# Performance work log

Measured on AMD Instinct MI355X. Metric: run time of the kernel, lower is better.

The kernel has to match this reference:

```python
import jax, jax.numpy as jnp
import numpy as np

B, N, Mc, K = 8, 16384, 2048, 32
EMB = 256


def setup_inputs() -> dict:
    key = jax.random.key(0)
    ks = jax.random.split(key, 9)
    xyz = jax.random.normal(ks[0], (B, N, 3), dtype=jnp.float32)
    centers = jax.random.normal(ks[1], (B, Mc, 3), dtype=jnp.float32)
    idx_knn = jax.random.randint(ks[2], (B, Mc, K), 0, N, dtype=jnp.int32)
    # 1x1 conv weights == pointwise linear layers (out_ch, in_ch) + bias
    def kaiming(k, o, i):
        return jax.random.normal(k, (o, i), dtype=jnp.float32) * np.float32(np.sqrt(2.0 / i))
    W1, b1 = kaiming(ks[3], 64, 3), jnp.zeros((64,), jnp.float32)
    W2, b2 = kaiming(ks[4], 128, 64), jnp.zeros((128,), jnp.float32)
    W3, b3 = kaiming(ks[5], EMB, 128), jnp.zeros((EMB,), jnp.float32)
    return {"xyz": xyz, "centers": centers, "idx_knn": idx_knn,
            "W1": W1, "b1": b1, "W2": W2, "b2": b2, "W3": W3, "b3": b3}


def reference(xyz, centers, idx_knn, W1, b1, W2, b2, W3, b3):
    # gather KNN neighbors: (B, M, K, 3)
    neigh = jnp.take_along_axis(xyz[:, None, :, :], idx_knn[..., None], axis=2)
    local = neigh - centers[:, :, None, :]          # center-subtract
    # 1x1 convs are pointwise linears over the channel dim
    h = jax.nn.relu(jnp.einsum('bmkc,oc->bmko', local, W1) + b1)
    h = jax.nn.relu(jnp.einsum('bmkc,oc->bmko', h, W2) + b2)
    h = jnp.einsum('bmkc,oc->bmko', h, W3) + b3      # (B, M, K, EMB)
    return jnp.max(h, axis=2)                        # max over K -> (B, M, EMB)
```

## Files before the change

### kernel.cpp

```cpp
#include <hip/hip_runtime.h>
#include <hip/hip_bf16.h>


typedef __attribute__((ext_vector_type(8))) short bf16x8;
typedef __attribute__((ext_vector_type(4))) float f32x4v;

constexpr int Bn = 8, Nn = 16384, Mn = 2048, Kn = 32, EMB = 256;
constexpr int G = 2;
constexpr int ROWS = G * Kn;

__device__ __forceinline__ unsigned pk2(float a, float b) {
    float2 f; f.x = a; f.y = b;
    __hip_bfloat162 h = __float22bfloat162_rn(f);
    return *(unsigned*)&h;
}

__device__ __forceinline__ bf16x8 pack8(const float* v) {
    unsigned u0 = pk2(v[0], v[1]), u1 = pk2(v[2], v[3]);
    unsigned u2 = pk2(v[4], v[5]), u3 = pk2(v[6], v[7]);
    uint4 u = make_uint4(u0, u1, u2, u3);
    return *(bf16x8*)&u;
}

__global__ __launch_bounds__(256) void pe_pack(
    const float* __restrict__ W2, const float* __restrict__ W3,
    uint4* __restrict__ ws)
{
    int gid = blockIdx.x * 256 + threadIdx.x;
    if (gid < 1024) {
        int e = gid, l = e & 63;
        int kt = (e >> 6) & 1, ct = (e >> 7) & 1, w = e >> 8;
        int q = l >> 4, n = l & 15;
        int ch = w * 32 + ct * 16 + n;
        const float* p = W2 + ch * 64 + kt * 32 + q * 8;
        float t[8];
        *(float4*)&t[0] = *(const float4*)p;
        *(float4*)&t[4] = *(const float4*)(p + 4);
        bf16x8 v = pack8(t);
        ws[e] = *(uint4*)&v;
    } else if (gid < 5120) {
        int e = gid - 1024, l = e & 63;
        int kt = (e >> 6) & 3, ct = (e >> 8) & 3, w = e >> 10;
        int q = l >> 4, n = l & 15;
        int ch = w * 64 + ct * 16 + n;
        const float* p = W3 + ch * 128 + kt * 32 + q * 8;
        float t[8];
        *(float4*)&t[0] = *(const float4*)p;
        *(float4*)&t[4] = *(const float4*)(p + 4);
        bf16x8 v = pack8(t);
        ws[1024 + e] = *(uint4*)&v;
    }
}

__global__ __launch_bounds__(256, 4) void pe_mfma(
    const float* __restrict__ xyz,
    const float* __restrict__ centers,
    const int*   __restrict__ idx,
    const float* __restrict__ W1,
    const float* __restrict__ b1,
    const float* __restrict__ b2,
    const float* __restrict__ b3,
    const uint4* __restrict__ wsf,
    float*       __restrict__ out)
{
    __shared__ uint4 h1v[ROWS * 64 * 2 / 16];
    __shared__ uint4 h2v[ROWS * 128 * 2 / 16];

    const int tid = threadIdx.x;
    const int w   = tid >> 6;
    const int l   = tid & 63;
    const int q   = l >> 4;
    const int n   = l & 15;
    const int bm0 = blockIdx.x * G;

    bf16x8 B2f[2][2];
    float4 bb2[2];
    const int ch0 = w * 32 + q * 4;
    #pragma unroll
    for (int ct = 0; ct < 2; ++ct) {
        bb2[ct] = *(const float4*)&b2[ch0 + ct * 16];
        #pragma unroll
        for (int kt = 0; kt < 2; ++kt) {
            uint4 u = wsf[((w * 2 + ct) * 2 + kt) * 64 + l];
            B2f[ct][kt] = *(bf16x8*)&u;
        }
    }
    bf16x8 B3f[4][4];  float b3v[4];
    #pragma unroll
    for (int ct = 0; ct < 4; ++ct) {
        b3v[ct] = b3[w * 64 + ct * 16 + n];
        #pragma unroll
        for (int kt = 0; kt < 4; ++kt) {
            uint4 u = wsf[1024 + ((w * 4 + ct) * 4 + kt) * 64 + l];
            B3f[ct][kt] = *(bf16x8*)&u;
        }
    }

    const int r64 = tid & 63;
    {
        int bm = bm0 + (r64 >> 5);
        int bb = bm >> 11;
        int id = idx[(size_t)bm * Kn + (r64 & 31)];
        const float* p = xyz + ((size_t)bb * Nn + id) * 3;
        const float* c = centers + (size_t)bm * 3;
        float lx = p[0] - c[0], ly = p[1] - c[1], lz = p[2] - c[2];

        const int o4b = __builtin_amdgcn_readfirstlane((tid >> 6) * 4);
        float h[16];
        #pragma unroll
        for (int i = 0; i < 4; ++i) {
            const float4* Wp = (const float4*)(W1 + (o4b + i) * 12);
            float4 wa = Wp[0], wb = Wp[1], wc = Wp[2];
            float4 bb4 = *(const float4*)(b1 + (o4b + i) * 4);
            h[4*i+0] = fmaxf(bb4.x + lx*wa.x + ly*wa.y + lz*wa.z, 0.f);
            h[4*i+1] = fmaxf(bb4.y + lx*wa.w + ly*wb.x + lz*wb.y, 0.f);
            h[4*i+2] = fmaxf(bb4.z + lx*wb.z + ly*wb.w + lz*wc.x, 0.f);
            h[4*i+3] = fmaxf(bb4.w + lx*wc.y + ly*wc.z + lz*wc.w, 0.f);
        }
        const int T = r64 >> 4, r = r64 & 15, j0 = (tid >> 6) * 2;
        #pragma unroll
        for (int jj = 0; jj < 2; ++jj) {
            bf16x8 v = pack8(&h[8 * jj]);
            h1v[T * 128 + (j0 + jj) * 16 + r] = *(uint4*)&v;
        }
    }
    __syncthreads();

    {
        ushort* h2s = (ushort*)h2v;
        #pragma unroll
        for (int rt = 0; rt < G * 2; ++rt) {
            uint4 a0u = h1v[rt * 128 + q * 16 + n];
            uint4 a1u = h1v[rt * 128 + (4 + q) * 16 + n];
            bf16x8 A0 = *(bf16x8*)&a0u, A1 = *(bf16x8*)&a1u;
            #pragma unroll
            for (int ct = 0; ct < 2; ++ct) {
                int ch = ch0 + ct * 16;
                f32x4v c0 = {0.f, 0.f, 0.f, 0.f};
                c0 = __builtin_amdgcn_mfma_f32_16x16x32_bf16(B2f[ct][0], A0, c0, 0, 0, 0);
                c0 = __builtin_amdgcn_mfma_f32_16x16x32_bf16(B2f[ct][1], A1, c0, 0, 0, 0);
                unsigned p0 = pk2(fmaxf(c0[0] + bb2[ct].x, 0.f),
                                  fmaxf(c0[1] + bb2[ct].y, 0.f));
                unsigned p1 = pk2(fmaxf(c0[2] + bb2[ct].z, 0.f),
                                  fmaxf(c0[3] + bb2[ct].w, 0.f));
                uint2 pk; pk.x = p0; pk.y = p1;
                *(uint2*)&h2s[rt * 2048 + (ch >> 3) * 128 + n * 8 + (ch & 7)] = pk;
            }
        }
    }
    __syncthreads();

    {
        #pragma unroll
        for (int g = 0; g < G; ++g) {
            bf16x8 Ae[4], Ao[4];
            #pragma unroll
            for (int kt = 0; kt < 4; ++kt) {
                uint4 ae = h2v[(2*g)   * 256 + (kt * 4 + q) * 16 + n];
                uint4 ao = h2v[(2*g+1) * 256 + (kt * 4 + q) * 16 + n];
                Ae[kt] = *(bf16x8*)&ae;
                Ao[kt] = *(bf16x8*)&ao;
            }
            #pragma unroll
            for (int ct = 0; ct < 4; ++ct) {
                f32x4v Ce = {0.f, 0.f, 0.f, 0.f};
                f32x4v Co = {0.f, 0.f, 0.f, 0.f};
                #pragma unroll
                for (int kt = 0; kt < 4; ++kt) {
                    Ce = __builtin_amdgcn_mfma_f32_16x16x32_bf16(Ae[kt], B3f[ct][kt], Ce, 0, 0, 0);
                    Co = __builtin_amdgcn_mfma_f32_16x16x32_bf16(Ao[kt], B3f[ct][kt], Co, 0, 0, 0);
                }
                float v = fmaxf(fmaxf(fmaxf(Ce[0], Co[0]), fmaxf(Ce[1], Co[1])),
                                fmaxf(fmaxf(Ce[2], Co[2]), fmaxf(Ce[3], Co[3])));
                v = fmaxf(v, __shfl_xor(v, 16));
                v = fmaxf(v, __shfl_xor(v, 32));
                if (q == 0) {
                    out[(size_t)(bm0 + g) * EMB + w * 64 + ct * 16 + n] = v + b3v[ct];
                }
            }
        }
    }
}

extern "C" void kernel_launch(void* const* d_in, const int* in_sizes, int n_in,
                              void* d_out, int out_size, void* d_ws, size_t ws_size,
                              hipStream_t stream) {
    const float* xyz     = (const float*)d_in[0];
    const float* centers = (const float*)d_in[1];
    const int*   idx     = (const int*)  d_in[2];
    const float* W1      = (const float*)d_in[3];
    const float* b1      = (const float*)d_in[4];
    const float* W2      = (const float*)d_in[5];
    const float* b2      = (const float*)d_in[6];
    const float* W3      = (const float*)d_in[7];
    const float* b3      = (const float*)d_in[8];
    float*       out     = (float*)d_out;
    uint4*       ws      = (uint4*)d_ws;

    pe_pack<<<20, 256, 0, stream>>>(W2, W3, ws);
    pe_mfma<<<(Bn * Mn) / G, 256, 0, stream>>>(
        xyz, centers, idx, W1, b1, b2, b3, ws, out);
}
```

Baseline: 124.1 us.

## Stream W3 fragments from global inside loop to cut registers and raise occupancy

Stops preloading all 16 W3 MFMA B-fragments and the b3 values into registers at kernel start. Each output tile now loads its four fragments from the packed workspace inside a non-unrolled loop, and the launch bound is raised from 4 to 6 waves per SIMD. The goal is to lower VGPR pressure so more blocks stay resident and latency is hidden better. In exchange, W3 is reloaded from global/L2 for every group and channel tile, and serialized loops expose load latency before each MFMA chain.

```diff
diff --git a/kernel.cpp b/kernel.cpp
--- a/kernel.cpp
+++ b/kernel.cpp
@@ -52,7 +52,7 @@
     }
 }
 
-__global__ __launch_bounds__(256, 4) void pe_mfma(
+__global__ __launch_bounds__(256, 6) void pe_mfma(
     const float* __restrict__ xyz,
     const float* __restrict__ centers,
     const int*   __restrict__ idx,
@@ -83,16 +83,6 @@
         for (int kt = 0; kt < 2; ++kt) {
             uint4 u = wsf[((w * 2 + ct) * 2 + kt) * 64 + l];
             B2f[ct][kt] = *(bf16x8*)&u;
-        }
-    }
-    bf16x8 B3f[4][4];  float b3v[4];
-    #pragma unroll
-    for (int ct = 0; ct < 4; ++ct) {
-        b3v[ct] = b3[w * 64 + ct * 16 + n];
-        #pragma unroll
-        for (int kt = 0; kt < 4; ++kt) {
-            uint4 u = wsf[1024 + ((w * 4 + ct) * 4 + kt) * 64 + l];
-            B3f[ct][kt] = *(bf16x8*)&u;
         }
     }
 
@@ -151,7 +141,7 @@
     __syncthreads();
 
     {
-        #pragma unroll
+        #pragma unroll 1
         for (int g = 0; g < G; ++g) {
             bf16x8 Ae[4], Ao[4];
             #pragma unroll
@@ -161,21 +151,27 @@
                 Ae[kt] = *(bf16x8*)&ae;
                 Ao[kt] = *(bf16x8*)&ao;
             }
-            #pragma unroll
+            #pragma unroll 1
             for (int ct = 0; ct < 4; ++ct) {
+                const uint4* bp = &wsf[1024 + (w * 4 + ct) * 256 + l];
+                uint4 u0 = bp[0], u1 = bp[64], u2 = bp[128], u3 = bp[192];
                 f32x4v Ce = {0.f, 0.f, 0.f, 0.f};
                 f32x4v Co = {0.f, 0.f, 0.f, 0.f};
-                #pragma unroll
-                for (int kt = 0; kt < 4; ++kt) {
-                    Ce = __builtin_amdgcn_mfma_f32_16x16x32_bf16(Ae[kt], B3f[ct][kt], Ce, 0, 0, 0);
-                    Co = __builtin_amdgcn_mfma_f32_16x16x32_bf16(Ao[kt], B3f[ct][kt], Co, 0, 0, 0);
-                }
+                Ce = __builtin_amdgcn_mfma_f32_16x16x32_bf16(Ae[0], *(bf16x8*)&u0, Ce, 0, 0, 0);
+                Co = __builtin_amdgcn_mfma_f32_16x16x32_bf16(Ao[0], *(bf16x8*)&u0, Co, 0, 0, 0);
+                Ce = __builtin_amdgcn_mfma_f32_16x16x32_bf16(Ae[1], *(bf16x8*)&u1, Ce, 0, 0, 0);
+                Co = __builtin_amdgcn_mfma_f32_16x16x32_bf16(Ao[1], *(bf16x8*)&u1, Co, 0, 0, 0);
+                Ce = __builtin_amdgcn_mfma_f32_16x16x32_bf16(Ae[2], *(bf16x8*)&u2, Ce, 0, 0, 0);
+                Co = __builtin_amdgcn_mfma_f32_16x16x32_bf16(Ao[2], *(bf16x8*)&u2, Co, 0, 0, 0);
+                Ce = __builtin_amdgcn_mfma_f32_16x16x32_bf16(Ae[3], *(bf16x8*)&u3, Ce, 0, 0, 0);
+                Co = __builtin_amdgcn_mfma_f32_16x16x32_bf16(Ao[3], *(bf16x8*)&u3, Co, 0, 0, 0);
                 float v = fmaxf(fmaxf(fmaxf(Ce[0], Co[0]), fmaxf(Ce[1], Co[1])),
                                 fmaxf(fmaxf(Ce[2], Co[2]), fmaxf(Ce[3], Co[3])));
                 v = fmaxf(v, __shfl_xor(v, 16));
                 v = fmaxf(v, __shfl_xor(v, 32));
                 if (q == 0) {
-                    out[(size_t)(bm0 + g) * EMB + w * 64 + ct * 16 + n] = v + b3v[ct];
+                    out[(size_t)(bm0 + g) * EMB + w * 64 + ct * 16 + n] =
+                        v + b3[w * 64 + ct * 16 + n];
                 }
             }
         }
```

New measurement: 131.8 us. 6.2% more time.
